# Performance work log

Measured on AMD Instinct MI355X. Metric: run time of the kernel, lower is better.

The kernel has to match this reference:

```python
import jax, jax.numpy as jnp
import numpy as np

B, T, C = 4, 2048, 1024
H = 16
HD = C // H  # head_dim = 64


def setup_inputs() -> dict:
    key = jax.random.key(0)
    k1, k2, k3 = jax.random.split(key, 3)
    x = jax.random.normal(k1, (B, T, C), dtype=jnp.float32)
    # nn.Linear weights stored as (out_features, in_features); y = x @ W.T
    w_qkv = jax.random.normal(k2, (3 * C, C), dtype=jnp.float32) * (1.0 / np.sqrt(C))
    w_out = jax.random.normal(k3, (C, C), dtype=jnp.float32) * (1.0 / np.sqrt(C))
    return {"x": x, "w_qkv": w_qkv, "w_out": w_out}


def reference(x, w_qkv, w_out):
    Bb, Tt, Cc = x.shape
    qkv = jnp.einsum('btc,oc->bto', x, w_qkv)  # (B,T,3C)
    q, k, v = jnp.split(qkv, 3, axis=2)
    # (B,T,H,HD) -> (B,H,T,HD)
    q = q.reshape(Bb, Tt, H, HD).transpose(0, 2, 1, 3)
    k = k.reshape(Bb, Tt, H, HD).transpose(0, 2, 1, 3)
    v = v.reshape(Bb, Tt, H, HD).transpose(0, 2, 1, 3)
    scores = jnp.einsum('bhqd,bhkd->bhqk', q, k) / jnp.sqrt(jnp.float32(HD))
    causal = jnp.tril(jnp.ones((Tt, Tt), dtype=bool))  # True = keep
    scores = jnp.where(causal[None, None], scores, jnp.float32(-jnp.inf))
    weights = jax.nn.softmax(scores, axis=-1)
    att = jnp.einsum('bhqk,bhkd->bhqd', weights, v)  # (B,H,T,HD)
    att = att.transpose(0, 2, 1, 3).reshape(Bb, Tt, Cc)
    return jnp.einsum('btc,oc->bto', att, w_out)
```

## Files before the change

kernel.cpp:

```cpp
#include <hip/hip_runtime.h>
#include <hip/hip_bf16.h>

#define B_   4
#define T_   2048
#define C_   1024
#define H_   16
#define HD_  64
#define M_   8192
#define N1_  3072
#define N2_  1024

typedef __attribute__((ext_vector_type(8))) short bf16x8;
typedef __attribute__((ext_vector_type(4))) float f32x4;

static __device__ __forceinline__ unsigned short f2bf(float f) {
  union { float f; unsigned u; } cv; cv.f = f;
  unsigned u = cv.u;
  return (unsigned short)((u + 0x7FFFu + ((u >> 16) & 1u)) >> 16);
}

static __device__ __forceinline__ float exp2_fast(float x) {
  float r;
  asm("v_exp_f32 %0, %1" : "=v"(r) : "v"(x));
  return r;
}

static __device__ __forceinline__ unsigned cvt_pk_bf16(float lo, float hi) {
  unsigned r;
  asm("v_cvt_pk_bf16_f32 %0, %1, %2" : "=v"(r) : "v"(lo), "v"(hi));
  return r;
}

#define AS1 __attribute__((address_space(1)))
#define AS3 __attribute__((address_space(3)))
static __device__ __forceinline__ void gload_lds16(const void* g, void* l) {
  __builtin_amdgcn_global_load_lds((const AS1 void*)g, (AS3 void*)l, 16, 0, 0);
}

#define N4_X  (M_ * C_ / 4)
#define N4_WQ (N1_ * C_ / 4)
#define N4_WO (N2_ * C_ / 4)
__global__ void cast_all_kernel(const float* __restrict__ x, const float* __restrict__ wq,
                                const float* __restrict__ wo,
                                unsigned short* __restrict__ xb, unsigned short* __restrict__ wqb,
                                unsigned short* __restrict__ wob) {
  int stride = gridDim.x * blockDim.x;
  for (int i = blockIdx.x * blockDim.x + threadIdx.x; i < N4_X + N4_WQ + N4_WO; i += stride) {
    const float* src; unsigned short* dst; int j;
    if (i < N4_X)            { src = x;  dst = xb;  j = i; }
    else if (i < N4_X + N4_WQ) { src = wq; dst = wqb; j = i - N4_X; }
    else                     { src = wo; dst = wob; j = i - N4_X - N4_WQ; }
    f32x4 v = ((const f32x4*)src)[j];
    ushort4 o;
    o.x = f2bf(v[0]); o.y = f2bf(v[1]); o.z = f2bf(v[2]); o.w = f2bf(v[3]);
    ((ushort4*)dst)[j] = o;
  }
}

__global__ __launch_bounds__(256, 3) void gemm_qkv(
    const unsigned short* __restrict__ Xb,
    const unsigned short* __restrict__ Wb,
    unsigned short* __restrict__ Qb,
    unsigned short* __restrict__ Kb,
    unsigned short* __restrict__ Vtb)
{
  __shared__ __align__(16) unsigned short As[3][128 * 32];
  __shared__ __align__(16) unsigned short Bs[3][128 * 32];
  const int tid  = threadIdx.x;
  const int lane = tid & 63;
  const int wave = tid >> 6;
  const int wr = wave >> 1, wc = wave & 1;
  const int g = lane >> 4, q4 = lane & 15;
  const int row0 = blockIdx.x * 128;
  const int col0 = blockIdx.y * 128;
  const int NT = C_ / 32;

  auto stage = [&](int kt) {
    const int buf = kt % 3;
    const int k0 = kt * 32;
    #pragma unroll
    for (int i = 0; i < 2; ++i) {
      int cb = wave * 128 + i * 64;
      int c  = cb + lane;
      int r  = c >> 2;
      int j  = (c & 3) ^ ((r >> 1) & 3);
      gload_lds16(Xb + (size_t)(row0 + r) * C_ + k0 + j * 8, (char*)As[buf] + cb * 16);
      gload_lds16(Wb + (size_t)(col0 + r) * C_ + k0 + j * 8, (char*)Bs[buf] + cb * 16);
    }
  };

  f32x4 zero = {0.f, 0.f, 0.f, 0.f};
  f32x4 acc[4][4];
  for (int i = 0; i < 4; ++i) for (int j = 0; j < 4; ++j) acc[i][j] = zero;

  auto ktile = [&](int buf) {
    bf16x8 a[4], b[4];
    #pragma unroll
    for (int im = 0; im < 4; ++im) {
      int row = wr * 64 + im * 16 + q4;
      a[im] = *(const bf16x8*)((const char*)As[buf] + row * 64 + ((g ^ ((row >> 1) & 3)) * 16));
    }
    #pragma unroll
    for (int in_ = 0; in_ < 4; ++in_) {
      int row = wc * 64 + in_ * 16 + q4;
      b[in_] = *(const bf16x8*)((const char*)Bs[buf] + row * 64 + ((g ^ ((row >> 1) & 3)) * 16));
    }
    __builtin_amdgcn_s_setprio(1);
    #pragma unroll
    for (int im = 0; im < 4; ++im)
      #pragma unroll
      for (int in_ = 0; in_ < 4; ++in_)
        acc[im][in_] = __builtin_amdgcn_mfma_f32_16x16x32_bf16(a[im], b[in_], acc[im][in_], 0, 0, 0);
    __builtin_amdgcn_s_setprio(0);
  };

  stage(0); stage(1);
  for (int kt = 0; kt < NT - 1; ++kt) {
    asm volatile("s_waitcnt vmcnt(4)" ::: "memory");
    __builtin_amdgcn_s_barrier();
    __builtin_amdgcn_sched_barrier(0);
    if (kt + 2 < NT) stage(kt + 2);
    ktile(kt % 3);
  }
  asm volatile("s_waitcnt vmcnt(0)" ::: "memory");
  __builtin_amdgcn_s_barrier();
  __builtin_amdgcn_sched_barrier(0);
  ktile((NT - 1) % 3);

  const float SC = 0.125f * 1.44269504f;
  #pragma unroll
  for (int im = 0; im < 4; ++im) {
    #pragma unroll
    for (int in_ = 0; in_ < 4; ++in_) {
      f32x4 v = acc[im][in_];
      int col = col0 + wc * 64 + in_ * 16 + q4;
      int which = col >> 10;
      int cc = col & 1023;
      int h = cc >> 6, d = cc & 63;
      int r0 = row0 + wr * 64 + im * 16 + g * 4;
      int bb = r0 >> 11, t0 = r0 & 2047;
      if (which == 2) {
        uint2 pk;
        pk.x = cvt_pk_bf16(v[0], v[1]);
        pk.y = cvt_pk_bf16(v[2], v[3]);
        *(uint2*)(Vtb + (((size_t)(bb * 16 + h)) * 64 + d) * T_ + t0) = pk;
      } else {
        unsigned short* dst = (which == 0) ? Qb : Kb;
        float sc = (which == 0) ? SC : 1.f;
        #pragma unroll
        for (int rg = 0; rg < 4; ++rg)
          dst[(((size_t)(bb * 16 + h)) * T_ + t0 + rg) * 64 + d] = f2bf(v[rg] * sc);
      }
    }
  }
}

__global__ __launch_bounds__(256, 3) void attn_kernel(
    const unsigned short* __restrict__ Qb,
    const unsigned short* __restrict__ Kb,
    const unsigned short* __restrict__ Vtb,
    unsigned short* __restrict__ Ob)
{
  __shared__ __align__(16) unsigned short Ks[2][64 * 64];
  __shared__ __align__(16) unsigned short Vs[2][64 * 64];
  __shared__ __align__(16) unsigned short Ps[4][32 * 64];
  const int tid  = threadIdx.x;
  const int lane = tid & 63;
  const int wave = tid >> 6;
  const int g = lane >> 4, q4 = lane & 15;
  const int bh = blockIdx.x;
  const int qt = 15 - blockIdx.y;
  const unsigned short* Qp = Qb  + (size_t)bh * T_ * 64;
  const unsigned short* Kp = Kb  + (size_t)bh * T_ * 64;
  const unsigned short* Vp = Vtb + (size_t)bh * 64 * T_;
  const int qb = qt * 128 + wave * 32;
  const int nT = 2 * qt + 2;
  const int nKeys = qb + 31;

  bf16x8 qf[2][2];
  #pragma unroll
  for (int qtl = 0; qtl < 2; ++qtl)
    #pragma unroll
    for (int ks = 0; ks < 2; ++ks)
      qf[qtl][ks] = *(const bf16x8*)(Qp + (size_t)(qb + qtl * 16 + q4) * 64 + ks * 32 + g * 8);

  bf16x8 ones;
  #pragma unroll
  for (int i = 0; i < 8; ++i) ones[i] = (short)0x3F80;

  f32x4 zero = {0.f, 0.f, 0.f, 0.f};
  f32x4 oacc[2][4], lacc[2];
  #pragma unroll
  for (int i = 0; i < 2; ++i) {
    lacc[i] = zero;
    #pragma unroll
    for (int jj = 0; jj < 4; ++jj) oacc[i][jj] = zero;
  }
  float m_run[2] = {-1e30f, -1e30f};
  const float THR = 10.0f;

  auto stage = [&](int t, int buf) {
    const int kv0 = t * 64;
    #pragma unroll
    for (int i = 0; i < 2; ++i) {
      int cb = wave * 128 + i * 64;
      int c  = cb + lane;
      int r  = c >> 3;
      int jx = (c & 7) ^ (r & 7);
      gload_lds16(Kp + (size_t)(kv0 + r) * 64 + jx * 8, (char*)Ks[buf] + cb * 16);
      gload_lds16(Vp + (size_t)r * T_ + kv0 + jx * 8,   (char*)Vs[buf] + cb * 16);
    }
  };

  stage(0, 0);
  for (int t = 0; t < nT; ++t) {
    asm volatile("s_waitcnt vmcnt(0)" ::: "memory");
    __builtin_amdgcn_s_barrier();
    __builtin_amdgcn_sched_barrier(0);
    if (t + 1 < nT) stage(t + 1, (t + 1) & 1);
    const int cur = t & 1;
    const int kv0 = t * 64;
    if (kv0 > nKeys) continue;

    f32x4 s[4][2];
    #pragma unroll
    for (int mt = 0; mt < 4; ++mt)
      #pragma unroll
      for (int qtl = 0; qtl < 2; ++qtl) s[mt][qtl] = zero;
    #pragma unroll
    for (int ks = 0; ks < 2; ++ks) {
      bf16x8 kf[4];
      #pragma unroll
      for (int mt = 0; mt < 4; ++mt) {
        int row = mt * 16 + q4;
        int byte = (row * 128 + (ks * 32 + g * 8) * 2) ^ ((row & 7) << 4);
        kf[mt] = *(const bf16x8*)((const char*)Ks[cur] + byte);
      }
      __builtin_amdgcn_s_setprio(1);
      #pragma unroll
      for (int mt = 0; mt < 4; ++mt)
        #pragma unroll
        for (int qtl = 0; qtl < 2; ++qtl)
          s[mt][qtl] = __builtin_amdgcn_mfma_f32_16x16x32_bf16(kf[mt], qf[qtl][ks], s[mt][qtl], 0, 0, 0);
      __builtin_amdgcn_s_setprio(0);
    }

    const bool needMask = (kv0 + 63 > qb);
    if (needMask) {
      #pragma unroll
      for (int mt = 0; mt < 4; ++mt)
        #pragma unroll
        for (int qtl = 0; qtl < 2; ++qtl)
          #pragma unroll
          for (int rg = 0; rg < 4; ++rg) {
            int key = kv0 + mt * 16 + g * 4 + rg;
            int qrow = qb + qtl * 16 + q4;
            s[mt][qtl][rg] = (key <= qrow) ? s[mt][qtl][rg] : -1e30f;
          }
    }
    float tmax[2];
    #pragma unroll
    for (int qtl = 0; qtl < 2; ++qtl) {
      float mm[4];
      #pragma unroll
      for (int mt = 0; mt < 4; ++mt)
        mm[mt] = fmaxf(fmaxf(s[mt][qtl][0], s[mt][qtl][1]),
                       fmaxf(s[mt][qtl][2], s[mt][qtl][3]));
      float tm = fmaxf(fmaxf(mm[0], mm[1]), fmaxf(mm[2], mm[3]));
      tm = fmaxf(tm, __shfl_xor(tm, 16, 64));
      tm = fmaxf(tm, __shfl_xor(tm, 32, 64));
      tmax[qtl] = tm;
    }
    if (!__all((tmax[0] <= m_run[0] + THR) & (tmax[1] <= m_run[1] + THR))) {
      #pragma unroll
      for (int qtl = 0; qtl < 2; ++qtl) {
        float mnew = fmaxf(m_run[qtl], tmax[qtl]);
        float alpha = exp2_fast(m_run[qtl] - mnew);
        m_run[qtl] = mnew;
        float al[4];
        #pragma unroll
        for (int rg = 0; rg < 4; ++rg) al[rg] = __shfl(alpha, g * 4 + rg, 64);
        #pragma unroll
        for (int dt = 0; dt < 4; ++dt)
          #pragma unroll
          for (int rg = 0; rg < 4; ++rg) oacc[qtl][dt][rg] *= al[rg];
        #pragma unroll
        for (int rg = 0; rg < 4; ++rg) lacc[qtl][rg] *= al[rg];
      }
    }
    #pragma unroll
    for (int qtl = 0; qtl < 2; ++qtl)
      #pragma unroll
      for (int mt = 0; mt < 4; ++mt) {
        float p0 = exp2_fast(s[mt][qtl][0] - m_run[qtl]);
        float p1 = exp2_fast(s[mt][qtl][1] - m_run[qtl]);
        float p2 = exp2_fast(s[mt][qtl][2] - m_run[qtl]);
        float p3 = exp2_fast(s[mt][qtl][3] - m_run[qtl]);
        uint2 pk;
        pk.x = cvt_pk_bf16(p0, p1);
        pk.y = cvt_pk_bf16(p2, p3);
        int row = qtl * 16 + q4;
        int byte = (row * 128 + (mt * 16 + g * 4) * 2) ^ ((row & 7) << 4);
        *(uint2*)((char*)Ps[wave] + byte) = pk;
      }
    #pragma unroll
    for (int ks = 0; ks < 2; ++ks) {
      bf16x8 pf[2], vf[4];
      #pragma unroll
      for (int qtl = 0; qtl < 2; ++qtl) {
        int row = qtl * 16 + q4;
        int byte = (row * 128 + (ks * 32 + g * 8) * 2) ^ ((row & 7) << 4);
        pf[qtl] = *(const bf16x8*)((const char*)Ps[wave] + byte);
      }
      #pragma unroll
      for (int dt = 0; dt < 4; ++dt) {
        int row = dt * 16 + q4;
        int byte = (row * 128 + (ks * 32 + g * 8) * 2) ^ ((row & 7) << 4);
        vf[dt] = *(const bf16x8*)((const char*)Vs[cur] + byte);
      }
      __builtin_amdgcn_s_setprio(1);
      #pragma unroll
      for (int qtl = 0; qtl < 2; ++qtl) {
        #pragma unroll
        for (int dt = 0; dt < 4; ++dt)
          oacc[qtl][dt] = __builtin_amdgcn_mfma_f32_16x16x32_bf16(pf[qtl], vf[dt], oacc[qtl][dt], 0, 0, 0);
        lacc[qtl] = __builtin_amdgcn_mfma_f32_16x16x32_bf16(pf[qtl], ones, lacc[qtl], 0, 0, 0);
      }
      __builtin_amdgcn_s_setprio(0);
    }
  }

  #pragma unroll
  for (int qtl = 0; qtl < 2; ++qtl) {
    #pragma unroll
    for (int dt = 0; dt < 4; ++dt) {
      #pragma unroll
      for (int rg = 0; rg < 4; ++rg) {
        int tq = qb + qtl * 16 + g * 4 + rg;
        int d = dt * 16 + q4;
        Ob[((size_t)bh * T_ + tq) * 64 + d] = f2bf(oacc[qtl][dt][rg] / lacc[qtl][rg]);
      }
    }
  }
}

__global__ __launch_bounds__(256, 3) void gemm_out(
    const unsigned short* __restrict__ Ob,
    const unsigned short* __restrict__ Wo,
    float* __restrict__ Out)
{
  __shared__ __align__(16) unsigned short As[3][128 * 32];
  __shared__ __align__(16) unsigned short Bs[3][128 * 32];
  const int tid  = threadIdx.x;
  const int lane = tid & 63;
  const int wave = tid >> 6;
  const int wr = wave >> 1, wc = wave & 1;
  const int g = lane >> 4, q4 = lane & 15;
  const int row0 = blockIdx.x * 128;
  const int col0 = blockIdx.y * 128;
  const int NT = C_ / 32;

  auto stage = [&](int kt) {
    const int buf = kt % 3;
    const int k0 = kt * 32;
    #pragma unroll
    for (int i = 0; i < 2; ++i) {
      int cb = wave * 128 + i * 64;
      int c  = cb + lane;
      int r  = c >> 2;
      int j  = (c & 3) ^ ((r >> 1) & 3);
      int rr = row0 + r;
      int cc = k0 + j * 8;
      const unsigned short* srcA =
          Ob + (((size_t)((rr >> 11) * 16 + (cc >> 6))) * T_ + (rr & 2047)) * 64 + (cc & 63);
      gload_lds16(srcA, (char*)As[buf] + cb * 16);
      gload_lds16(Wo + (size_t)(col0 + r) * C_ + cc, (char*)Bs[buf] + cb * 16);
    }
  };

  f32x4 zero = {0.f, 0.f, 0.f, 0.f};
  f32x4 acc[4][4];
  for (int i = 0; i < 4; ++i) for (int j = 0; j < 4; ++j) acc[i][j] = zero;

  auto ktile = [&](int buf) {
    bf16x8 a[4], b[4];
    #pragma unroll
    for (int im = 0; im < 4; ++im) {
      int row = wr * 64 + im * 16 + q4;
      a[im] = *(const bf16x8*)((const char*)As[buf] + row * 64 + ((g ^ ((row >> 1) & 3)) * 16));
    }
    #pragma unroll
    for (int in_ = 0; in_ < 4; ++in_) {
      int row = wc * 64 + in_ * 16 + q4;
      b[in_] = *(const bf16x8*)((const char*)Bs[buf] + row * 64 + ((g ^ ((row >> 1) & 3)) * 16));
    }
    __builtin_amdgcn_s_setprio(1);
    #pragma unroll
    for (int im = 0; im < 4; ++im)
      #pragma unroll
      for (int in_ = 0; in_ < 4; ++in_)
        acc[im][in_] = __builtin_amdgcn_mfma_f32_16x16x32_bf16(a[im], b[in_], acc[im][in_], 0, 0, 0);
    __builtin_amdgcn_s_setprio(0);
  };

  stage(0); stage(1);
  for (int kt = 0; kt < NT - 1; ++kt) {
    asm volatile("s_waitcnt vmcnt(4)" ::: "memory");
    __builtin_amdgcn_s_barrier();
    __builtin_amdgcn_sched_barrier(0);
    if (kt + 2 < NT) stage(kt + 2);
    ktile(kt % 3);
  }
  asm volatile("s_waitcnt vmcnt(0)" ::: "memory");
  __builtin_amdgcn_s_barrier();
  __builtin_amdgcn_sched_barrier(0);
  ktile((NT - 1) % 3);

  #pragma unroll
  for (int im = 0; im < 4; ++im)
    #pragma unroll
    for (int in_ = 0; in_ < 4; ++in_) {
      int col = col0 + wc * 64 + in_ * 16 + q4;
      #pragma unroll
      for (int rg = 0; rg < 4; ++rg) {
        int r = row0 + wr * 64 + im * 16 + g * 4 + rg;
        Out[(size_t)r * C_ + col] = acc[im][in_][rg];
      }
    }
}

extern "C" void kernel_launch(void* const* d_in, const int* in_sizes, int n_in,
                              void* d_out, int out_size, void* d_ws, size_t ws_size,
                              hipStream_t stream) {
  const float* x     = (const float*)d_in[0];
  const float* w_qkv = (const float*)d_in[1];
  const float* w_out = (const float*)d_in[2];
  float* out = (float*)d_out;
  char* ws = (char*)d_ws;
  unsigned short* xb  = (unsigned short*)(ws);
  unsigned short* wqb = (unsigned short*)(ws + 16777216);
  unsigned short* wob = (unsigned short*)(ws + 16777216 + 6291456);
  unsigned short* Qb  = (unsigned short*)(ws + 25165824);
  unsigned short* Kb  = (unsigned short*)(ws + 25165824 + 16777216);
  unsigned short* Vtb = (unsigned short*)(ws + 25165824 + 2 * 16777216);
  unsigned short* Ob  = (unsigned short*)(ws + 25165824 + 3 * 16777216);

  cast_all_kernel<<<2048, 256, 0, stream>>>(x, w_qkv, w_out, xb, wqb, wob);
  gemm_qkv<<<dim3(M_ / 128, N1_ / 128), 256, 0, stream>>>(xb, wqb, Qb, Kb, Vtb);
  attn_kernel<<<dim3(B_ * H_, 16), 256, 0, stream>>>(Qb, Kb, Vtb, Ob);
  gemm_out<<<dim3(M_ / 128, N2_ / 128), 256, 0, stream>>>(Ob, wob, out);
}
```

Baseline: 160.2 us.

## Retile QKV GEMM to 256x256 blocks with 8 waves and quadrant-interleaved pipeline

Rewrites the QKV projection GEMM to use 256x256 output tiles, 512 threads and a 64-wide K step. Each tile is split into 128-row and 128-column halves that are loaded and computed quadrant by quadrant, so the next K tile's loads overlap with MFMA work. A row-XOR swizzle is used in LDS to avoid bank conflicts. The aim is more data reuse per byte loaded and fewer barriers per FLOP, at the cost of 128 KB of LDS, fewer blocks (384) on 256 CUs and higher register pressure.

```diff
diff --git a/kernel.cpp b/kernel.cpp
--- a/kernel.cpp
+++ b/kernel.cpp
@@ -57,99 +57,181 @@
   }
 }
 
-__global__ __launch_bounds__(256, 3) void gemm_qkv(
+__global__ __launch_bounds__(512, 2) void gemm_qkv(
     const unsigned short* __restrict__ Xb,
     const unsigned short* __restrict__ Wb,
     unsigned short* __restrict__ Qb,
     unsigned short* __restrict__ Kb,
     unsigned short* __restrict__ Vtb)
 {
-  __shared__ __align__(16) unsigned short As[3][128 * 32];
-  __shared__ __align__(16) unsigned short Bs[3][128 * 32];
+  __shared__ __align__(16) unsigned short As[2][256 * 64];
+  __shared__ __align__(16) unsigned short Bs[2][256 * 64];
   const int tid  = threadIdx.x;
   const int lane = tid & 63;
   const int wave = tid >> 6;
-  const int wr = wave >> 1, wc = wave & 1;
+  const int rowgrp = wave >> 1;
+  const int colgrp = wave & 1;
   const int g = lane >> 4, q4 = lane & 15;
-  const int row0 = blockIdx.x * 128;
-  const int col0 = blockIdx.y * 128;
-  const int NT = C_ / 32;
-
-  auto stage = [&](int kt) {
-    const int buf = kt % 3;
-    const int k0 = kt * 32;
-    #pragma unroll
-    for (int i = 0; i < 2; ++i) {
-      int cb = wave * 128 + i * 64;
-      int c  = cb + lane;
-      int r  = c >> 2;
-      int j  = (c & 3) ^ ((r >> 1) & 3);
-      gload_lds16(Xb + (size_t)(row0 + r) * C_ + k0 + j * 8, (char*)As[buf] + cb * 16);
-      gload_lds16(Wb + (size_t)(col0 + r) * C_ + k0 + j * 8, (char*)Bs[buf] + cb * 16);
+  const int row0 = blockIdx.x * 256;
+  const int col0 = blockIdx.y * 256;
+  const int NT = C_ / 64;
+
+  const int cb0 = wave * 128;
+  const int cb1 = wave * 128 + 64;
+  const int c0 = cb0 + lane, c1 = cb1 + lane;
+  const int r0s = c0 >> 3, j0 = (c0 & 7) ^ (r0s & 7);
+  const int r1s = c1 >> 3, j1 = (c1 & 7) ^ (r1s & 7);
+  const unsigned short* xs0 = Xb + (size_t)(row0 + r0s) * C_ + j0 * 8;
+  const unsigned short* xs1 = Xb + (size_t)(row0 + r1s) * C_ + j1 * 8;
+  const unsigned short* ws0 = Wb + (size_t)(col0 + r0s) * C_ + j0 * 8;
+  const unsigned short* ws1 = Wb + (size_t)(col0 + r1s) * C_ + j1 * 8;
+
+  auto stage = [&](int t, int h, int isB) {
+    const int buf = t & 1;
+    const size_t hoff = (size_t)h * 128 * C_;
+    const int k0 = t * 64;
+    const unsigned short* s0 = (isB ? ws0 : xs0) + hoff + k0;
+    const unsigned short* s1 = (isB ? ws1 : xs1) + hoff + k0;
+    char* dbase = (char*)(isB ? Bs[buf] : As[buf]) + h * 1024 * 16;
+    gload_lds16(s0, dbase + cb0 * 16);
+    gload_lds16(s1, dbase + cb1 * 16);
+  };
+
+  bf16x8 aA[2][2], aB[2][2], bb[4][2];
+  auto readA = [&](bf16x8 (&a)[2][2], int buf, int h) {
+    #pragma unroll
+    for (int mt = 0; mt < 2; ++mt) {
+      int row = h * 128 + rowgrp * 32 + mt * 16 + q4;
+      #pragma unroll
+      for (int ks = 0; ks < 2; ++ks) {
+        int byte = (row * 128 + (ks * 32 + g * 8) * 2) ^ ((row & 7) << 4);
+        a[mt][ks] = *(const bf16x8*)((const char*)As[buf] + byte);
+      }
+    }
+  };
+  auto readB = [&](int buf, int h) {
+    #pragma unroll
+    for (int nt = 0; nt < 4; ++nt) {
+      int row = h * 128 + colgrp * 64 + nt * 16 + q4;
+      #pragma unroll
+      for (int ks = 0; ks < 2; ++ks) {
+        int byte = (row * 128 + (ks * 32 + g * 8) * 2) ^ ((row & 7) << 4);
+        bb[nt][ks] = *(const bf16x8*)((const char*)Bs[buf] + byte);
+      }
     }
   };
 
   f32x4 zero = {0.f, 0.f, 0.f, 0.f};
-  f32x4 acc[4][4];
-  for (int i = 0; i < 4; ++i) for (int j = 0; j < 4; ++j) acc[i][j] = zero;
-
-  auto ktile = [&](int buf) {
-    bf16x8 a[4], b[4];
-    #pragma unroll
-    for (int im = 0; im < 4; ++im) {
-      int row = wr * 64 + im * 16 + q4;
-      a[im] = *(const bf16x8*)((const char*)As[buf] + row * 64 + ((g ^ ((row >> 1) & 3)) * 16));
-    }
-    #pragma unroll
-    for (int in_ = 0; in_ < 4; ++in_) {
-      int row = wc * 64 + in_ * 16 + q4;
-      b[in_] = *(const bf16x8*)((const char*)Bs[buf] + row * 64 + ((g ^ ((row >> 1) & 3)) * 16));
-    }
+  f32x4 acc00[2][4], acc10[2][4], acc11[2][4], acc01[2][4];
+  #pragma unroll
+  for (int m = 0; m < 2; ++m)
+    #pragma unroll
+    for (int n = 0; n < 4; ++n) { acc00[m][n] = zero; acc10[m][n] = zero; acc11[m][n] = zero; acc01[m][n] = zero; }
+
+  auto mfma16 = [&](f32x4 (&ac)[2][4], bf16x8 (&a)[2][2]) {
     __builtin_amdgcn_s_setprio(1);
     #pragma unroll
-    for (int im = 0; im < 4; ++im)
-      #pragma unroll
-      for (int in_ = 0; in_ < 4; ++in_)
-        acc[im][in_] = __builtin_amdgcn_mfma_f32_16x16x32_bf16(a[im], b[in_], acc[im][in_], 0, 0, 0);
+    for (int mt = 0; mt < 2; ++mt)
+      #pragma unroll
+      for (int nt = 0; nt < 4; ++nt)
+        #pragma unroll
+        for (int ks = 0; ks < 2; ++ks)
+          ac[mt][nt] = __builtin_amdgcn_mfma_f32_16x16x32_bf16(a[mt][ks], bb[nt][ks], ac[mt][nt], 0, 0, 0);
     __builtin_amdgcn_s_setprio(0);
   };
 
-  stage(0); stage(1);
-  for (int kt = 0; kt < NT - 1; ++kt) {
-    asm volatile("s_waitcnt vmcnt(4)" ::: "memory");
-    __builtin_amdgcn_s_barrier();
-    __builtin_amdgcn_sched_barrier(0);
-    if (kt + 2 < NT) stage(kt + 2);
-    ktile(kt % 3);
-  }
+  stage(0, 0, 0); stage(0, 0, 1); stage(0, 1, 0); stage(0, 1, 1);
   asm volatile("s_waitcnt vmcnt(0)" ::: "memory");
   __builtin_amdgcn_s_barrier();
   __builtin_amdgcn_sched_barrier(0);
-  ktile((NT - 1) % 3);
+
+  for (int t = 0; t < NT - 1; ++t) {
+    const int buf = t & 1;
+    readA(aA, buf, 0);
+    readB(buf, 0);
+    stage(t + 1, 0, 0);
+    asm volatile("s_waitcnt lgkmcnt(0)" ::: "memory");
+    __builtin_amdgcn_sched_barrier(0);
+    mfma16(acc00, aA);
+    asm volatile("s_waitcnt vmcnt(4)" ::: "memory");
+    __builtin_amdgcn_s_barrier();
+    __builtin_amdgcn_sched_barrier(0);
+    readA(aB, buf, 1);
+    stage(t + 1, 0, 1);
+    asm volatile("s_waitcnt lgkmcnt(0)" ::: "memory");
+    __builtin_amdgcn_sched_barrier(0);
+    mfma16(acc10, aB);
+    asm volatile("s_waitcnt vmcnt(4)" ::: "memory");
+    __builtin_amdgcn_s_barrier();
+    __builtin_amdgcn_sched_barrier(0);
+    readB(buf, 1);
+    stage(t + 1, 1, 0);
+    asm volatile("s_waitcnt lgkmcnt(0)" ::: "memory");
+    __builtin_amdgcn_sched_barrier(0);
+    mfma16(acc11, aB);
+    asm volatile("s_waitcnt vmcnt(4)" ::: "memory");
+    __builtin_amdgcn_s_barrier();
+    __builtin_amdgcn_sched_barrier(0);
+    stage(t + 1, 1, 1);
+    mfma16(acc01, aA);
+    asm volatile("s_waitcnt vmcnt(4)" ::: "memory");
+    __builtin_amdgcn_s_barrier();
+    __builtin_amdgcn_sched_barrier(0);
+  }
+  {
+    const int buf = (NT - 1) & 1;
+    readA(aA, buf, 0);
+    readB(buf, 0);
+    asm volatile("s_waitcnt lgkmcnt(0)" ::: "memory");
+    __builtin_amdgcn_sched_barrier(0);
+    mfma16(acc00, aA);
+    asm volatile("s_waitcnt vmcnt(2)" ::: "memory");
+    __builtin_amdgcn_s_barrier();
+    __builtin_amdgcn_sched_barrier(0);
+    readA(aB, buf, 1);
+    asm volatile("s_waitcnt lgkmcnt(0)" ::: "memory");
+    __builtin_amdgcn_sched_barrier(0);
+    mfma16(acc10, aB);
+    asm volatile("s_waitcnt vmcnt(0)" ::: "memory");
+    __builtin_amdgcn_s_barrier();
+    __builtin_amdgcn_sched_barrier(0);
+    readB(buf, 1);
+    asm volatile("s_waitcnt lgkmcnt(0)" ::: "memory");
+    __builtin_amdgcn_sched_barrier(0);
+    mfma16(acc11, aB);
+    mfma16(acc01, aA);
+  }
 
   const float SC = 0.125f * 1.44269504f;
   #pragma unroll
-  for (int im = 0; im < 4; ++im) {
-    #pragma unroll
-    for (int in_ = 0; in_ < 4; ++in_) {
-      f32x4 v = acc[im][in_];
-      int col = col0 + wc * 64 + in_ * 16 + q4;
-      int which = col >> 10;
-      int cc = col & 1023;
-      int h = cc >> 6, d = cc & 63;
-      int r0 = row0 + wr * 64 + im * 16 + g * 4;
-      int bb = r0 >> 11, t0 = r0 & 2047;
-      if (which == 2) {
-        uint2 pk;
-        pk.x = cvt_pk_bf16(v[0], v[1]);
-        pk.y = cvt_pk_bf16(v[2], v[3]);
-        *(uint2*)(Vtb + (((size_t)(bb * 16 + h)) * 64 + d) * T_ + t0) = pk;
-      } else {
-        unsigned short* dst = (which == 0) ? Qb : Kb;
-        float sc = (which == 0) ? SC : 1.f;
-        #pragma unroll
-        for (int rg = 0; rg < 4; ++rg)
-          dst[(((size_t)(bb * 16 + h)) * T_ + t0 + rg) * 64 + d] = f2bf(v[rg] * sc);
+  for (int qr = 0; qr < 2; ++qr) {
+    #pragma unroll
+    for (int qc = 0; qc < 2; ++qc) {
+      #pragma unroll
+      for (int mt = 0; mt < 2; ++mt) {
+        #pragma unroll
+        for (int nt = 0; nt < 4; ++nt) {
+          f32x4 v = (qr == 0) ? ((qc == 0) ? acc00[mt][nt] : acc01[mt][nt])
+                              : ((qc == 0) ? acc10[mt][nt] : acc11[mt][nt]);
+          int col = col0 + qc * 128 + colgrp * 64 + nt * 16 + q4;
+          int which = col >> 10;
+          int cc = col & 1023;
+          int h = cc >> 6, d = cc & 63;
+          int r0 = row0 + qr * 128 + rowgrp * 32 + mt * 16 + g * 4;
+          int bb_ = r0 >> 11, t0 = r0 & 2047;
+          if (which == 2) {
+            uint2 pk;
+            pk.x = cvt_pk_bf16(v[0], v[1]);
+            pk.y = cvt_pk_bf16(v[2], v[3]);
+            *(uint2*)(Vtb + (((size_t)(bb_ * 16 + h)) * 64 + d) * T_ + t0) = pk;
+          } else {
+            unsigned short* dst = (which == 0) ? Qb : Kb;
+            float sc = (which == 0) ? SC : 1.f;
+            #pragma unroll
+            for (int rg = 0; rg < 4; ++rg)
+              dst[(((size_t)(bb_ * 16 + h)) * T_ + t0 + rg) * 64 + d] = f2bf(v[rg] * sc);
+          }
+        }
       }
     }
   }
@@ -446,7 +528,7 @@
   unsigned short* Ob  = (unsigned short*)(ws + 25165824 + 3 * 16777216);
 
   cast_all_kernel<<<2048, 256, 0, stream>>>(x, w_qkv, w_out, xb, wqb, wob);
-  gemm_qkv<<<dim3(M_ / 128, N1_ / 128), 256, 0, stream>>>(xb, wqb, Qb, Kb, Vtb);
+  gemm_qkv<<<dim3(M_ / 256, N1_ / 256), 512, 0, stream>>>(xb, wqb, Qb, Kb, Vtb);
   attn_kernel<<<dim3(B_ * H_, 16), 256, 0, stream>>>(Qb, Kb, Vtb, Ob);
   gemm_out<<<dim3(M_ / 128, N2_ / 128), 256, 0, stream>>>(Ob, wob, out);
 }
```

Measured after the change: 168.6 us. 5.2% more time.

## Fuse fp32-to-bf16 cast of x into QKV GEMM A-tile loading

Applied to the files above, without the earlier changes.

Removes the separate conversion of the activation x to bf16. The QKV GEMM now loads fp32 x into registers, converts it with packed bf16 instructions, and writes the result to LDS, while the weight tiles still use direct global-to-LDS loads. The main loop is restructured into a two-step unrolled pipeline with explicit vmcnt/lgkmcnt waits and double register buffers. This saves a full write and re-read of the 16MB bf16 x, but each GEMM block now reads fp32 x. Since 24 column blocks reread x, that doubles A-side global traffic and adds register pressure and VALU work inside the GEMM.

```diff
diff --git a/kernel.cpp b/kernel.cpp
--- a/kernel.cpp
+++ b/kernel.cpp
@@ -37,19 +37,15 @@
   __builtin_amdgcn_global_load_lds((const AS1 void*)g, (AS3 void*)l, 16, 0, 0);
 }
 
-#define N4_X  (M_ * C_ / 4)
 #define N4_WQ (N1_ * C_ / 4)
 #define N4_WO (N2_ * C_ / 4)
-__global__ void cast_all_kernel(const float* __restrict__ x, const float* __restrict__ wq,
-                                const float* __restrict__ wo,
-                                unsigned short* __restrict__ xb, unsigned short* __restrict__ wqb,
-                                unsigned short* __restrict__ wob) {
+__global__ void cast_w_kernel(const float* __restrict__ wq, const float* __restrict__ wo,
+                              unsigned short* __restrict__ wqb, unsigned short* __restrict__ wob) {
   int stride = gridDim.x * blockDim.x;
-  for (int i = blockIdx.x * blockDim.x + threadIdx.x; i < N4_X + N4_WQ + N4_WO; i += stride) {
+  for (int i = blockIdx.x * blockDim.x + threadIdx.x; i < N4_WQ + N4_WO; i += stride) {
     const float* src; unsigned short* dst; int j;
-    if (i < N4_X)            { src = x;  dst = xb;  j = i; }
-    else if (i < N4_X + N4_WQ) { src = wq; dst = wqb; j = i - N4_X; }
-    else                     { src = wo; dst = wob; j = i - N4_X - N4_WQ; }
+    if (i < N4_WQ) { src = wq; dst = wqb; j = i; }
+    else           { src = wo; dst = wob; j = i - N4_WQ; }
     f32x4 v = ((const f32x4*)src)[j];
     ushort4 o;
     o.x = f2bf(v[0]); o.y = f2bf(v[1]); o.z = f2bf(v[2]); o.w = f2bf(v[3]);
@@ -58,7 +54,7 @@
 }
 
 __global__ __launch_bounds__(256, 3) void gemm_qkv(
-    const unsigned short* __restrict__ Xb,
+    const float* __restrict__ Xf,
     const unsigned short* __restrict__ Wb,
     unsigned short* __restrict__ Qb,
     unsigned short* __restrict__ Kb,
@@ -75,7 +71,41 @@
   const int col0 = blockIdx.y * 128;
   const int NT = C_ / 32;
 
-  auto stage = [&](int kt) {
+  const int cA0 = wave * 128 + lane;
+  const int cA1 = wave * 128 + 64 + lane;
+  const int rA0 = cA0 >> 2, qA0 = cA0 & 3;
+  const int rA1 = cA1 >> 2, qA1 = cA1 & 3;
+  const float* xsrc0 = Xf + (size_t)(row0 + rA0) * C_ + qA0 * 8;
+  const float* xsrc1 = Xf + (size_t)(row0 + rA1) * C_ + qA1 * 8;
+  const int dstA0 = rA0 * 64 + ((qA0 ^ ((rA0 >> 1) & 3)) * 16);
+  const int dstA1 = rA1 * 64 + ((qA1 ^ ((rA1 >> 1) & 3)) * 16);
+
+  f32x4 bkA0[4], bkA1[4];
+
+  auto issueA = [&](int t, f32x4* bk) {
+    const float* s0 = xsrc0 + t * 32;
+    const float* s1 = xsrc1 + t * 32;
+    bk[0] = ((const f32x4*)s0)[0];
+    bk[1] = ((const f32x4*)s0)[1];
+    bk[2] = ((const f32x4*)s1)[0];
+    bk[3] = ((const f32x4*)s1)[1];
+  };
+  auto writeA = [&](int t, const f32x4* bk) {
+    const int buf = t % 3;
+    uint4 w0, w1;
+    w0.x = cvt_pk_bf16(bk[0][0], bk[0][1]);
+    w0.y = cvt_pk_bf16(bk[0][2], bk[0][3]);
+    w0.z = cvt_pk_bf16(bk[1][0], bk[1][1]);
+    w0.w = cvt_pk_bf16(bk[1][2], bk[1][3]);
+    w1.x = cvt_pk_bf16(bk[2][0], bk[2][1]);
+    w1.y = cvt_pk_bf16(bk[2][2], bk[2][3]);
+    w1.z = cvt_pk_bf16(bk[3][0], bk[3][1]);
+    w1.w = cvt_pk_bf16(bk[3][2], bk[3][3]);
+    *(uint4*)((char*)As[buf] + dstA0) = w0;
+    *(uint4*)((char*)As[buf] + dstA1) = w1;
+  };
+
+  auto stageW = [&](int kt) {
     const int buf = kt % 3;
     const int k0 = kt * 32;
     #pragma unroll
@@ -84,7 +114,6 @@
       int c  = cb + lane;
       int r  = c >> 2;
       int j  = (c & 3) ^ ((r >> 1) & 3);
-      gload_lds16(Xb + (size_t)(row0 + r) * C_ + k0 + j * 8, (char*)As[buf] + cb * 16);
       gload_lds16(Wb + (size_t)(col0 + r) * C_ + k0 + j * 8, (char*)Bs[buf] + cb * 16);
     }
   };
@@ -114,18 +143,41 @@
     __builtin_amdgcn_s_setprio(0);
   };
 
-  stage(0); stage(1);
-  for (int kt = 0; kt < NT - 1; ++kt) {
-    asm volatile("s_waitcnt vmcnt(4)" ::: "memory");
-    __builtin_amdgcn_s_barrier();
-    __builtin_amdgcn_sched_barrier(0);
-    if (kt + 2 < NT) stage(kt + 2);
+  #define SB0()   __builtin_amdgcn_sched_barrier(0)
+  #define VMC(n)  asm volatile("s_waitcnt vmcnt(" #n ")" ::: "memory")
+  #define LGKM0() asm volatile("s_waitcnt lgkmcnt(0)" ::: "memory")
+
+  issueA(0, bkA0); SB0();
+  issueA(1, bkA1); SB0();
+  stageW(0); stageW(1); SB0();
+  VMC(8);
+  writeA(0, bkA0);
+
+  for (int kt = 0; kt < NT - 2; kt += 2) {
+    VMC(2); LGKM0();
+    __builtin_amdgcn_s_barrier(); SB0();
+    issueA(kt + 2, bkA0); SB0();
+    stageW(kt + 2); SB0();
+    writeA(kt + 1, bkA1);
     ktile(kt % 3);
-  }
-  asm volatile("s_waitcnt vmcnt(0)" ::: "memory");
-  __builtin_amdgcn_s_barrier();
-  __builtin_amdgcn_sched_barrier(0);
+    VMC(2); LGKM0();
+    __builtin_amdgcn_s_barrier(); SB0();
+    issueA(kt + 3, bkA1); SB0();
+    stageW(kt + 3); SB0();
+    writeA(kt + 2, bkA0);
+    ktile((kt + 1) % 3);
+  }
+  VMC(2); LGKM0();
+  __builtin_amdgcn_s_barrier(); SB0();
+  writeA(NT - 1, bkA1);
+  ktile((NT - 2) % 3);
+  VMC(0); LGKM0();
+  __builtin_amdgcn_s_barrier(); SB0();
   ktile((NT - 1) % 3);
+
+  #undef SB0
+  #undef VMC
+  #undef LGKM0
 
   const float SC = 0.125f * 1.44269504f;
   #pragma unroll
@@ -437,7 +489,6 @@
   const float* w_out = (const float*)d_in[2];
   float* out = (float*)d_out;
   char* ws = (char*)d_ws;
-  unsigned short* xb  = (unsigned short*)(ws);
   unsigned short* wqb = (unsigned short*)(ws + 16777216);
   unsigned short* wob = (unsigned short*)(ws + 16777216 + 6291456);
   unsigned short* Qb  = (unsigned short*)(ws + 25165824);
@@ -445,8 +496,8 @@
   unsigned short* Vtb = (unsigned short*)(ws + 25165824 + 2 * 16777216);
   unsigned short* Ob  = (unsigned short*)(ws + 25165824 + 3 * 16777216);
 
-  cast_all_kernel<<<2048, 256, 0, stream>>>(x, w_qkv, w_out, xb, wqb, wob);
-  gemm_qkv<<<dim3(M_ / 128, N1_ / 128), 256, 0, stream>>>(xb, wqb, Qb, Kb, Vtb);
+  cast_w_kernel<<<1024, 256, 0, stream>>>(w_qkv, w_out, wqb, wob);
+  gemm_qkv<<<dim3(M_ / 128, N1_ / 128), 256, 0, stream>>>(x, wqb, Qb, Kb, Vtb);
   attn_kernel<<<dim3(B_ * H_, 16), 256, 0, stream>>>(Qb, Kb, Vtb, Ob);
   gemm_out<<<dim3(M_ / 128, N2_ / 128), 256, 0, stream>>>(Ob, wob, out);
 }
```

Measured after the change: 162.2 us. No clear change (+1.3%).
